# Kernel optimization log

Measured on AMD Instinct MI355X. Metric: run time of the kernel, lower is better.

The kernel has to match this reference:

```python
import jax, jax.numpy as jnp
import numpy as np

B, S, D = 8, 2048, 768

def setup_inputs() -> dict:
    key = jax.random.key(0)
    k1, k2, k3, k4 = jax.random.split(key, 4)
    x = jax.random.normal(k1, (B, S, D), dtype=jnp.float32)
    # torch Linear stores weight as [out, in] and computes x @ W^T; we store
    # pre-transposed [in, out] matrices so forward is x @ W.
    scale = 1.0 / np.sqrt(D)
    wq = jax.random.normal(k2, (D, D), dtype=jnp.float32) * scale
    wk = jax.random.normal(k3, (D, D), dtype=jnp.float32) * scale
    wv = jax.random.normal(k4, (D, D), dtype=jnp.float32) * scale
    return {"x": x, "wq": wq, "wk": wk, "wv": wv}

def reference(x, wq, wk, wv):
    d_out = wq.shape[1]
    q = jnp.einsum('bsd,de->bse', x, wq)
    k = jnp.einsum('bsd,de->bse', x, wk)
    v = jnp.einsum('bsd,de->bse', x, wv)
    # causal scores: note source scales by sqrt(d_out), not per-head dim
    scores = jnp.einsum('bqe,bke->bqk', q, k) / jnp.sqrt(jnp.float32(d_out))
    S_len = x.shape[1]
    causal = jnp.tril(jnp.ones((S_len, S_len), dtype=bool))  # True = keep
    scores = jnp.where(causal[None, :, :], scores, -jnp.inf)
    attn = jax.nn.softmax(scores, axis=-1)
    # dropout rate = 0.0 -> identity
    out = jnp.einsum('bqk,bke->bqe', attn, v)
    return out
```

## Files before the change

### kernel.cpp

```cpp
#include <hip/hip_runtime.h>
#include <hip/hip_bf16.h>

#define DI 768
#define SS 2048
#define QK_ELEMS ((size_t)16384 * 768)

typedef float f32x4 __attribute__((ext_vector_type(4)));
typedef short s16x8 __attribute__((ext_vector_type(8)));
typedef short s16x4 __attribute__((ext_vector_type(4)));

static __device__ __forceinline__ unsigned short f2bf(float f) {
    union { float f; unsigned int u; } a; a.f = f;
    unsigned int r = (a.u + 0x7FFFu + ((a.u >> 16) & 1u)) >> 16;
    return (unsigned short)r;
}

#define GLOAD_LDS16(SRC, DST) \
    __builtin_amdgcn_global_load_lds((const __attribute__((address_space(1))) unsigned int*)(SRC), \
                                     (__attribute__((address_space(3))) unsigned int*)(DST), 16, 0, 0)

__global__ __launch_bounds__(256) void conv_kernel(
    const float* __restrict__ x, unsigned short* __restrict__ xb)
{
    const size_t i = ((size_t)blockIdx.x * 256 + threadIdx.x) * 8;
    float4 a = *(const float4*)(x + i);
    float4 c = *(const float4*)(x + i + 4);
    ushort4 u0, u1;
    u0.x = f2bf(a.x); u0.y = f2bf(a.y); u0.z = f2bf(a.z); u0.w = f2bf(a.w);
    u1.x = f2bf(c.x); u1.y = f2bf(c.y); u1.z = f2bf(c.z); u1.w = f2bf(c.w);
    *(ushort4*)(xb + i) = u0;
    *(ushort4*)(xb + i + 4) = u1;
}

__global__ __launch_bounds__(256) void convw_kernel(
    const float* __restrict__ wq, const float* __restrict__ wk,
    const float* __restrict__ wv, unsigned short* __restrict__ wtb)
{
    __shared__ float tile[64][65];
    const int which = blockIdx.z;
    const float* w = (which == 0) ? wq : (which == 1) ? wk : wv;
    unsigned short* o = wtb + (size_t)which * DI * DI;
    const int k0 = blockIdx.x * 64, n0 = blockIdx.y * 64;
    const int tid = threadIdx.x;
    #pragma unroll
    for (int i = 0; i < 16; ++i) {
        int idx = tid + i * 256;
        int rr = idx >> 6, cc = idx & 63;
        tile[rr][cc] = w[(size_t)(k0 + rr) * DI + n0 + cc];
    }
    __syncthreads();
    #pragma unroll
    for (int i = 0; i < 16; ++i) {
        int idx = tid + i * 256;
        int rr = idx >> 6, cc = idx & 63;
        o[(size_t)(n0 + rr) * DI + k0 + cc] = f2bf(tile[cc][rr]);
    }
}

__global__ __launch_bounds__(256) void proj_kernel(
    const unsigned short* __restrict__ xb, const unsigned short* __restrict__ wtb,
    unsigned short* __restrict__ ws)
{
    __shared__ unsigned short As[128 * 32];
    __shared__ unsigned short Bs[128 * 32];

    const int which = blockIdx.z;
    const unsigned short* wt = wtb + (size_t)which * DI * DI;
    const int n0 = blockIdx.x * 128;
    const int m0 = blockIdx.y * 128;
    const int tid = threadIdx.x;
    const int lane = tid & 63, wid = tid >> 6;
    const int wr = wid >> 1, wc = wid & 1;
    const int r = lane & 15, g = lane >> 4;

    const int arow_l = lane >> 2;
    const int asrc_l = (((lane & 3) * 16) ^ ((arow_l & 1) << 5)) >> 1;

    f32x4 acc[4][4];
    #pragma unroll
    for (int i = 0; i < 4; ++i)
        #pragma unroll
        for (int j = 0; j < 4; ++j) acc[i][j] = (f32x4){0.f, 0.f, 0.f, 0.f};

    for (int k0 = 0; k0 < DI; k0 += 32) {
        #pragma unroll
        for (int ii = 0; ii < 2; ++ii) {
            const int idx = wid * 2 + ii;
            GLOAD_LDS16(xb + (size_t)(m0 + idx * 16 + arow_l) * DI + k0 + asrc_l,
                        &As[idx * 512]);
            GLOAD_LDS16(wt + (size_t)(n0 + idx * 16 + arow_l) * DI + k0 + asrc_l,
                        &Bs[idx * 512]);
        }
        __syncthreads();
        s16x8 af[4], bfr[4];
        #pragma unroll
        for (int fr = 0; fr < 4; ++fr) {
            const int arow = wr * 64 + fr * 16 + r;
            af[fr] = *(const s16x8*)((const char*)As + arow * 64 + ((g * 16) ^ ((arow & 1) << 5)));
        }
        #pragma unroll
        for (int cf = 0; cf < 4; ++cf) {
            const int brow = wc * 64 + cf * 16 + r;
            bfr[cf] = *(const s16x8*)((const char*)Bs + brow * 64 + ((g * 16) ^ ((brow & 1) << 5)));
        }
        #pragma unroll
        for (int fr = 0; fr < 4; ++fr)
            #pragma unroll
            for (int cf = 0; cf < 4; ++cf)
                acc[fr][cf] = __builtin_amdgcn_mfma_f32_16x16x32_bf16(af[fr], bfr[cf], acc[fr][cf], 0, 0, 0);
        __syncthreads();
    }

    const float scale = (which == 0) ? 0.03608439182435161f : 1.0f;
    if (which < 2) {
        unsigned short* O = ws + (size_t)which * QK_ELEMS;
        #pragma unroll
        for (int fr = 0; fr < 4; ++fr)
            #pragma unroll
            for (int cf = 0; cf < 4; ++cf) {
                int row = m0 + wr * 64 + fr * 16 + g * 4;
                int col = n0 + wc * 64 + cf * 16 + r;
                #pragma unroll
                for (int jj = 0; jj < 4; ++jj) {
                    int rr = row + jj;
                    int cc = col ^ ((rr & 7) << 3);
                    O[(size_t)rr * DI + cc] = f2bf(acc[fr][cf][jj] * scale);
                }
            }
    } else {
        unsigned short* O = ws + 2 * QK_ELEMS;
        #pragma unroll
        for (int fr = 0; fr < 4; ++fr)
            #pragma unroll
            for (int cf = 0; cf < 4; ++cf) {
                int row = m0 + wr * 64 + fr * 16 + g * 4;
                int bb = row >> 11;
                int st = (row & 2047) >> 4;
                int et = ((n0 + wc * 64) >> 4) + cf;
                ushort4 pk;
                pk.x = f2bf(acc[fr][cf][0]); pk.y = f2bf(acc[fr][cf][1]);
                pk.z = f2bf(acc[fr][cf][2]); pk.w = f2bf(acc[fr][cf][3]);
                *(ushort4*)&O[(((size_t)bb * 128 + st) * 48 + et) * 256 + lane * 4] = pk;
            }
    }
}

__global__ __launch_bounds__(512, 1) void attn_kernel(
    const unsigned short* __restrict__ ws, float* __restrict__ out)
{
    __shared__ unsigned short Ks[64 * 768];
    __shared__ unsigned short Qs[32 * 768];
    __shared__ unsigned short P_lds[2048];
    __shared__ float redm[128];

    const int id = blockIdx.x;
    const int b = id & 7;
    const int a = id >> 3;
    const int tid = threadIdx.x;
    const int wid = tid >> 6, lane = tid & 63;
    const int qsel = wid >> 2;
    const int wv = wid & 3;
    const int r = lane & 15, g = lane >> 4;
    const int et0 = wid * 6;
    const int rw = wv * 16 + r;
    const int swz = (r & 7) << 4;

    const unsigned short* Qb = ws + (size_t)b * SS * DI;
    const unsigned short* Kb = ws + QK_ELEMS + (size_t)b * SS * DI;
    const unsigned short* Vf = ws + 2 * QK_ELEMS + (size_t)b * 128 * 48 * 256;
    float* Ob = out + (size_t)b * SS * DI;
    const char* KsB = (const char*)Ks;
    const char* QsB = (const char*)Qs;

#define STAGEK(KT) do { \
        const size_t sbase_ = (size_t)(KT) * 64 * DI; \
        _Pragma("unroll") \
        for (int i_ = 0; i_ < 12; ++i_) { \
            const int idx_ = wid * 12 + i_; \
            GLOAD_LDS16(Kb + sbase_ + idx_ * 512 + lane * 8, &Ks[idx_ * 512]); \
        } \
    } while (0)

#define RAWBAR() do { \
        asm volatile("s_waitcnt lgkmcnt(0)" ::: "memory"); \
        __builtin_amdgcn_sched_barrier(0); \
        __builtin_amdgcn_s_barrier(); \
        __builtin_amdgcn_sched_barrier(0); \
    } while (0)

    for (int pp = 0; pp < 2; ++pp) {
        const int jbase = pp ? (126 - 2 * a) : (2 * a);
        const int q0 = (jbase + qsel) * 16;
        const int nt0 = (jbase * 16 + 79) >> 6;
        const int ntmax = ((jbase + 1) * 16 + 79) >> 6;
        const int nt_own = qsel ? ntmax : nt0;

        {
            const size_t qsb = (size_t)jbase * 16 * DI;
            #pragma unroll
            for (int i_ = 0; i_ < 6; ++i_) {
                const int idx_ = wid * 6 + i_;
                GLOAD_LDS16(Qb + qsb + idx_ * 512 + lane * 8, &Qs[idx_ * 512]);
            }
        }
        STAGEK(0);

        f32x4 acc[2][6];
        #pragma unroll
        for (int qs = 0; qs < 2; ++qs)
            #pragma unroll
            for (int cf = 0; cf < 6; ++cf) acc[qs][cf] = (f32x4){0.f, 0.f, 0.f, 0.f};
        float m0 = -1e30f, m1 = -1e30f, lp = 0.f;

        for (int kt = 0; kt < ntmax; ++kt) {
            const int k0 = kt * 64;
            const bool act0 = kt < nt0;
            const bool act_own = kt < nt_own;
            __syncthreads();

            s16x4 va[4][6];
            const size_t vbase = ((size_t)(k0 >> 4) * 48 + et0) * 256 + lane * 4;
            #pragma unroll
            for (int ks = 0; ks < 4; ++ks)
                #pragma unroll
                for (int cf = 0; cf < 6; ++cf)
                    va[ks][cf] = *(const s16x4*)(Vf + vbase + (size_t)ks * 48 * 256 + cf * 256);

            f32x4 s = {0.f, 0.f, 0.f, 0.f};
            if (act_own) {
                f32x4 sa = {0,0,0,0}, sb = {0,0,0,0};
                #pragma unroll
                for (int t = 0; t < 24; t += 2) {
                    const int c0 = (t * 64 + g * 16) ^ swz;
                    const int c1 = (t * 64 + 64 + g * 16) ^ swz;
                    s16x8 qa  = *(const s16x8*)(QsB + qsel * 24576 + r * 1536 + c0);
                    s16x8 qb2 = *(const s16x8*)(QsB + qsel * 24576 + r * 1536 + c1);
                    s16x8 ka  = *(const s16x8*)(KsB + rw * 1536 + c0);
                    s16x8 kb2 = *(const s16x8*)(KsB + rw * 1536 + c1);
                    sa = __builtin_amdgcn_mfma_f32_16x16x32_bf16(ka,  qa,  sa, 0, 0, 0);
                    sb = __builtin_amdgcn_mfma_f32_16x16x32_bf16(kb2, qb2, sb, 0, 0, 0);
                }
                #pragma unroll
                for (int jj = 0; jj < 4; ++jj) s[jj] = sa[jj] + sb[jj];
                if (k0 + 64 > q0) {
                    #pragma unroll
                    for (int jj = 0; jj < 4; ++jj)
                        if (k0 + 16 * wv + 4 * g + jj > q0 + r) s[jj] = -1e30f;
                }
                float v = fmaxf(fmaxf(s[0], s[1]), fmaxf(s[2], s[3]));
                v = fmaxf(v, __shfl_xor(v, 16));
                v = fmaxf(v, __shfl_xor(v, 32));
                if (lane < 16) redm[qsel * 64 + wv * 16 + lane] = v;
            }
            RAWBAR();

            if (kt + 1 < ntmax) STAGEK(kt + 1);

            {
                float vm1 = fmaxf(fmaxf(redm[64 + r], redm[80 + r]),
                                  fmaxf(redm[96 + r], redm[112 + r]));
                float vm0 = act0 ? fmaxf(fmaxf(redm[r], redm[16 + r]),
                                         fmaxf(redm[32 + r], redm[48 + r])) : -1e30f;
                bool need = __any(vm1 > m1 + 8.0f) || (act0 && __any(vm0 > m0 + 8.0f));
                if (need) {
                    const float mn0 = fmaxf(m0, vm0), mn1 = fmaxf(m1, vm1);
                    const float a0 = __expf(m0 - mn0), a1 = __expf(m1 - mn1);
                    m0 = mn0; m1 = mn1;
                    lp *= qsel ? a1 : a0;
                    float al0[4], al1[4];
                    #pragma unroll
                    for (int jj = 0; jj < 4; ++jj) {
                        al0[jj] = __shfl(a0, 4 * g + jj);
                        al1[jj] = __shfl(a1, 4 * g + jj);
                    }
                    #pragma unroll
                    for (int cf = 0; cf < 6; ++cf)
                        #pragma unroll
                        for (int jj = 0; jj < 4; ++jj) {
                            acc[0][cf][jj] *= al0[jj];
                            acc[1][cf][jj] *= al1[jj];
                        }
                }
                if (act_own) {
                    const float mo = qsel ? m1 : m0;
                    s16x4 pw;
                    #pragma unroll
                    for (int jj = 0; jj < 4; ++jj) {
                        float p = __expf(s[jj] - mo);
                        lp += p;
                        pw[jj] = (short)f2bf(p);
                    }
                    *(s16x4*)&P_lds[qsel * 1024 + wv * 256 + r * 16 + g * 4] = pw;
                }
            }
            RAWBAR();

            {
                s16x4 pa0[4], pa1[4];
                #pragma unroll
                for (int ks = 0; ks < 4; ++ks) {
                    pa0[ks] = *(const s16x4*)&P_lds[ks * 256 + r * 16 + g * 4];
                    pa1[ks] = *(const s16x4*)&P_lds[1024 + ks * 256 + r * 16 + g * 4];
                }
                if (act0) {
                    #pragma unroll
                    for (int cf = 0; cf < 6; ++cf)
                        #pragma unroll
                        for (int ks = 0; ks < 4; ++ks)
                            acc[0][cf] = __builtin_amdgcn_mfma_f32_16x16x16bf16_1k(pa0[ks], va[ks][cf], acc[0][cf], 0, 0, 0);
                }
                #pragma unroll
                for (int cf = 0; cf < 6; ++cf)
                    #pragma unroll
                    for (int ks = 0; ks < 4; ++ks)
                        acc[1][cf] = __builtin_amdgcn_mfma_f32_16x16x16bf16_1k(pa1[ks], va[ks][cf], acc[1][cf], 0, 0, 0);
            }
        }
        lp += __shfl_xor(lp, 16);
        lp += __shfl_xor(lp, 32);
        if (lane < 16) redm[qsel * 64 + wv * 16 + lane] = lp;
        __syncthreads();
        const float lt0 = redm[r] + redm[16 + r] + redm[32 + r] + redm[48 + r];
        const float lt1 = redm[64 + r] + redm[80 + r] + redm[96 + r] + redm[112 + r];
        const float li0 = 1.0f / lt0, li1 = 1.0f / lt1;
        float lv0[4], lv1[4];
        #pragma unroll
        for (int jj = 0; jj < 4; ++jj) {
            lv0[jj] = __shfl(li0, 4 * g + jj);
            lv1[jj] = __shfl(li1, 4 * g + jj);
        }
        #pragma unroll
        for (int cf = 0; cf < 6; ++cf)
            #pragma unroll
            for (int jj = 0; jj < 4; ++jj) {
                Ob[(size_t)(jbase * 16 + 4 * g + jj) * DI + wid * 96 + cf * 16 + r] = acc[0][cf][jj] * lv0[jj];
                Ob[(size_t)((jbase + 1) * 16 + 4 * g + jj) * DI + wid * 96 + cf * 16 + r] = acc[1][cf][jj] * lv1[jj];
            }
        __syncthreads();
    }
#undef STAGEK
#undef RAWBAR
}

extern "C" void kernel_launch(void* const* d_in, const int* in_sizes, int n_in,
                              void* d_out, int out_size, void* d_ws, size_t ws_size,
                              hipStream_t stream) {
    const float* x  = (const float*)d_in[0];
    const float* wq = (const float*)d_in[1];
    const float* wk = (const float*)d_in[2];
    const float* wv = (const float*)d_in[3];
    unsigned short* ws = (unsigned short*)d_ws;
    float* out = (float*)d_out;
    unsigned short* xb  = (unsigned short*)d_out;
    unsigned short* wtb = (unsigned short*)d_out + QK_ELEMS;

    conv_kernel<<<(int)(QK_ELEMS / (256 * 8)), 256, 0, stream>>>(x, xb);
    convw_kernel<<<dim3(12, 12, 3), 256, 0, stream>>>(wq, wk, wv, wtb);
    proj_kernel<<<dim3(6, 128, 3), 256, 0, stream>>>(xb, wtb, ws);
    attn_kernel<<<256, 512, 0, stream>>>(ws, out);
}
```

Before: 263.4 us.

## Load K fragments directly from global in MFMA layout, drop K LDS staging

The projection kernel now writes K in a fragment-tiled layout so each lane can load its MFMA operand straight from global memory. The attention kernel drops the 96KB K shared-memory buffer and its async staging, which cuts LDS use enough to allow two blocks per CU (launch bounds raised to 2). The V fragment loads are moved after the QK^T MFMAs. In exchange, K is read from global/L2 per wave without LDS reuse, and the prefetch overlap of the next K tile is lost.

After: 300.2 us. 1.14x slower.

```diff
diff --git a/kernel.cpp b/kernel.cpp
--- a/kernel.cpp
+++ b/kernel.cpp
@@ -111,9 +111,9 @@
         __syncthreads();
     }
 
-    const float scale = (which == 0) ? 0.03608439182435161f : 1.0f;
-    if (which < 2) {
-        unsigned short* O = ws + (size_t)which * QK_ELEMS;
+    if (which == 0) {
+        const float scale = 0.03608439182435161f;
+        unsigned short* O = ws;
         #pragma unroll
         for (int fr = 0; fr < 4; ++fr)
             #pragma unroll
@@ -125,6 +125,22 @@
                     int rr = row + jj;
                     int cc = col ^ ((rr & 7) << 3);
                     O[(size_t)rr * DI + cc] = f2bf(acc[fr][cf][jj] * scale);
+                }
+            }
+    } else if (which == 1) {
+        unsigned short* O = ws + QK_ELEMS;
+        #pragma unroll
+        for (int fr = 0; fr < 4; ++fr)
+            #pragma unroll
+            for (int cf = 0; cf < 4; ++cf) {
+                int row = m0 + wr * 64 + fr * 16 + g * 4;
+                int col = n0 + wc * 64 + cf * 16 + r;
+                const int dt = col >> 5, gf = (col >> 3) & 3, e = col & 7;
+                #pragma unroll
+                for (int jj = 0; jj < 4; ++jj) {
+                    int rr = row + jj;
+                    O[((size_t)(rr >> 4) * 24 + dt) * 512 + (rr & 15) * 8 + gf * 128 + e]
+                        = f2bf(acc[fr][cf][jj]);
                 }
             }
     } else {
@@ -145,10 +161,9 @@
     }
 }
 
-__global__ __launch_bounds__(512, 1) void attn_kernel(
+__global__ __launch_bounds__(512, 2) void attn_kernel(
     const unsigned short* __restrict__ ws, float* __restrict__ out)
 {
-    __shared__ unsigned short Ks[64 * 768];
     __shared__ unsigned short Qs[32 * 768];
     __shared__ unsigned short P_lds[2048];
     __shared__ float redm[128];
@@ -162,24 +177,13 @@
     const int wv = wid & 3;
     const int r = lane & 15, g = lane >> 4;
     const int et0 = wid * 6;
-    const int rw = wv * 16 + r;
     const int swz = (r & 7) << 4;
 
     const unsigned short* Qb = ws + (size_t)b * SS * DI;
-    const unsigned short* Kb = ws + QK_ELEMS + (size_t)b * SS * DI;
+    const unsigned short* Kf = ws + QK_ELEMS + (size_t)b * 128 * 24 * 512;
     const unsigned short* Vf = ws + 2 * QK_ELEMS + (size_t)b * 128 * 48 * 256;
     float* Ob = out + (size_t)b * SS * DI;
-    const char* KsB = (const char*)Ks;
     const char* QsB = (const char*)Qs;
-
-#define STAGEK(KT) do { \
-        const size_t sbase_ = (size_t)(KT) * 64 * DI; \
-        _Pragma("unroll") \
-        for (int i_ = 0; i_ < 12; ++i_) { \
-            const int idx_ = wid * 12 + i_; \
-            GLOAD_LDS16(Kb + sbase_ + idx_ * 512 + lane * 8, &Ks[idx_ * 512]); \
-        } \
-    } while (0)
 
 #define RAWBAR() do { \
         asm volatile("s_waitcnt lgkmcnt(0)" ::: "memory"); \
@@ -203,7 +207,7 @@
                 GLOAD_LDS16(Qb + qsb + idx_ * 512 + lane * 8, &Qs[idx_ * 512]);
             }
         }
-        STAGEK(0);
+        __syncthreads();
 
         f32x4 acc[2][6];
         #pragma unroll
@@ -216,27 +220,19 @@
             const int k0 = kt * 64;
             const bool act0 = kt < nt0;
             const bool act_own = kt < nt_own;
-            __syncthreads();
-
-            s16x4 va[4][6];
-            const size_t vbase = ((size_t)(k0 >> 4) * 48 + et0) * 256 + lane * 4;
-            #pragma unroll
-            for (int ks = 0; ks < 4; ++ks)
-                #pragma unroll
-                for (int cf = 0; cf < 6; ++cf)
-                    va[ks][cf] = *(const s16x4*)(Vf + vbase + (size_t)ks * 48 * 256 + cf * 256);
 
             f32x4 s = {0.f, 0.f, 0.f, 0.f};
             if (act_own) {
+                const unsigned short* kfr = Kf + (size_t)(kt * 4 + wv) * 12288 + lane * 8;
                 f32x4 sa = {0,0,0,0}, sb = {0,0,0,0};
                 #pragma unroll
                 for (int t = 0; t < 24; t += 2) {
+                    s16x8 ka  = *(const s16x8*)(kfr + t * 512);
+                    s16x8 kb2 = *(const s16x8*)(kfr + (t + 1) * 512);
                     const int c0 = (t * 64 + g * 16) ^ swz;
                     const int c1 = (t * 64 + 64 + g * 16) ^ swz;
                     s16x8 qa  = *(const s16x8*)(QsB + qsel * 24576 + r * 1536 + c0);
                     s16x8 qb2 = *(const s16x8*)(QsB + qsel * 24576 + r * 1536 + c1);
-                    s16x8 ka  = *(const s16x8*)(KsB + rw * 1536 + c0);
-                    s16x8 kb2 = *(const s16x8*)(KsB + rw * 1536 + c1);
                     sa = __builtin_amdgcn_mfma_f32_16x16x32_bf16(ka,  qa,  sa, 0, 0, 0);
                     sb = __builtin_amdgcn_mfma_f32_16x16x32_bf16(kb2, qb2, sb, 0, 0, 0);
                 }
@@ -247,14 +243,23 @@
                     for (int jj = 0; jj < 4; ++jj)
                         if (k0 + 16 * wv + 4 * g + jj > q0 + r) s[jj] = -1e30f;
                 }
+            }
+
+            s16x4 va[4][6];
+            const size_t vbase = ((size_t)(k0 >> 4) * 48 + et0) * 256 + lane * 4;
+            #pragma unroll
+            for (int ks = 0; ks < 4; ++ks)
+                #pragma unroll
+                for (int cf = 0; cf < 6; ++cf)
+                    va[ks][cf] = *(const s16x4*)(Vf + vbase + (size_t)ks * 48 * 256 + cf * 256);
+
+            if (act_own) {
                 float v = fmaxf(fmaxf(s[0], s[1]), fmaxf(s[2], s[3]));
                 v = fmaxf(v, __shfl_xor(v, 16));
                 v = fmaxf(v, __shfl_xor(v, 32));
                 if (lane < 16) redm[qsel * 64 + wv * 16 + lane] = v;
             }
             RAWBAR();
-
-            if (kt + 1 < ntmax) STAGEK(kt + 1);
 
             {
                 float vm1 = fmaxf(fmaxf(redm[64 + r], redm[80 + r]),
@@ -338,7 +343,6 @@
             }
         __syncthreads();
     }
-#undef STAGEK
 #undef RAWBAR
 }
 
```
